# Kernel optimization log

Measured on AMD Instinct MI355X. Metric: run time of the kernel, lower is better.

The kernel has to match this reference:

```python
import jax, jax.numpy as jnp
import numpy as np

FEAT = 64      # feature_dim
HEADS = 4      # n_head
LATENT = 256   # latent_dim
G = 128        # num graphs
NPG = 150      # nodes per graph (<=180 for one-hot positions)
N = G * NPG    # 19200 nodes
E = N * 12     # 230400 edges (excl. self loops)
POS = 180      # one-hot position classes
SLOPE = 0.2    # PyG GATConv leaky_relu negative slope


def gat_conv(x, src, dst, W, att_s, att_d, bias):
    """PyG GATConv (concat heads, self loops already appended to src/dst)."""
    n = x.shape[0]
    h = (x @ W).reshape(n, HEADS, FEAT)                 # [N,H,F]
    a_s = jnp.sum(h * att_s, axis=-1)                   # [N,H]
    a_d = jnp.sum(h * att_d, axis=-1)                   # [N,H]
    e = jax.nn.leaky_relu(a_s[src] + a_d[dst], SLOPE)   # [E,H] per-edge logits
    m = jax.ops.segment_max(e, dst, num_segments=n)     # segment softmax over dst
    ex = jnp.exp(e - m[dst])
    s = jax.ops.segment_sum(ex, dst, num_segments=n)
    alpha = ex / (s[dst] + 1e-16)
    out = jax.ops.segment_sum(h[src] * alpha[:, :, None], dst, num_segments=n)
    return out.reshape(n, HEADS * FEAT) + bias


def setup_inputs() -> dict:
    key = jax.random.key(0)
    ks = jax.random.split(key, 20)

    def p(k, shape, fan_in):
        return jax.random.normal(k, shape, jnp.float32) / np.sqrt(fan_in).astype(np.float32)

    z = jax.random.normal(ks[0], (G, LATENT), jnp.float32)
    src = jax.random.randint(ks[1], (E,), 0, N, jnp.int32)
    dst = (src + jax.random.randint(ks[2], (E,), 1, N, jnp.int32)) % N  # no self loops
    edge_index = jnp.stack([src, dst])
    batch = jnp.repeat(jnp.arange(G, dtype=jnp.int32), NPG)

    in1 = FEAT + POS
    in2 = FEAT * HEADS
    inp = dict(z=z, edge_index=edge_index, batch=batch, num_graphs=G)
    inp.update(
        W0=p(ks[3], (LATENT, FEAT), LATENT), b0=jnp.zeros(FEAT, jnp.float32),
        W1=p(ks[4], (in1, HEADS * FEAT), in1),
        as1=p(ks[5], (HEADS, FEAT), FEAT), ad1=p(ks[6], (HEADS, FEAT), FEAT),
        bb1=jnp.zeros(HEADS * FEAT, jnp.float32),
        W2=p(ks[7], (in2, HEADS * FEAT), in2),
        as2=p(ks[8], (HEADS, FEAT), FEAT), ad2=p(ks[9], (HEADS, FEAT), FEAT),
        bb2=jnp.zeros(HEADS * FEAT, jnp.float32),
        W3=p(ks[10], (in2, HEADS * FEAT), in2),
        as3=p(ks[11], (HEADS, FEAT), FEAT), ad3=p(ks[12], (HEADS, FEAT), FEAT),
        bb3=jnp.zeros(HEADS * FEAT, jnp.float32),
        Wg=p(ks[13], (in2, FEAT), in2), bg=jnp.zeros(FEAT, jnp.float32),
        Wf=p(ks[14], (FEAT, 5), FEAT), bf=jnp.zeros(5, jnp.float32),
    )
    return inp


def reference(z, edge_index, batch, num_graphs,
              W0, b0, W1, as1, ad1, bb1, W2, as2, ad2, bb2,
              W3, as3, ad3, bb3, Wg, bg, Wf, bf):
    n = batch.shape[0]
    x = z @ W0 + b0                                    # dec_feature_init
    x = x[batch]                                       # broadcast graph latent to nodes
    # node_order_within_batch (batch is sorted)
    counts = jax.ops.segment_sum(jnp.ones_like(batch), batch, num_segments=num_graphs)
    starts = jnp.cumsum(counts) - counts
    order = jnp.arange(n, dtype=batch.dtype) - starts[batch]
    pos = jax.nn.one_hot(order, POS, dtype=x.dtype)
    x = jax.nn.relu(jnp.concatenate([x, pos], axis=1))
    # GATConv adds self loops by default
    loops = jnp.arange(n, dtype=edge_index.dtype)
    src = jnp.concatenate([edge_index[0], loops])
    dst = jnp.concatenate([edge_index[1], loops])
    x = jax.nn.relu(gat_conv(x, src, dst, W1, as1, ad1, bb1))
    x = jax.nn.relu(gat_conv(x, src, dst, W2, as2, ad2, bb2))
    x = jax.nn.relu(gat_conv(x, src, dst, W3, as3, ad3, bb3))
    x = jax.nn.relu(x @ Wg + bg)                       # dec_geo
    return x @ Wf + bf                                 # fc_geo -> [N,5]
```

## Files before the change

kernel.cpp:

```cpp
#include <hip/hip_runtime.h>
#include <hip/hip_fp16.h>

#define GNUM 128
#define HEADS 4
#define FEAT 64
#define CH 256
#define LAT 256
#define SLOPE 0.2f
#define CAP 64
#define POSMAX 180

typedef _Float16 h16;
typedef __attribute__((ext_vector_type(4))) _Float16 half4;
typedef __attribute__((ext_vector_type(8))) _Float16 half8;
typedef __attribute__((ext_vector_type(4))) float floatx4;

__device__ __forceinline__ float lrelu(float x) { return fmaxf(x, SLOPE * x); }

__global__ __launch_bounds__(256) void k_setup(const int* __restrict__ batch, int* __restrict__ cnt,
                                               int* __restrict__ starts, int n,
                                               const float* __restrict__ W2, const float* __restrict__ W3,
                                               const float* __restrict__ Wg, h16* __restrict__ W2T,
                                               h16* __restrict__ W3T, h16* __restrict__ WgT,
                                               const float* __restrict__ z, const float* __restrict__ W0,
                                               const float* __restrict__ b0, const float* __restrict__ W1,
                                               const float* __restrict__ as1, const float* __restrict__ ad1,
                                               float* __restrict__ A, float* __restrict__ asg,
                                               float* __restrict__ adg, float* __restrict__ asp,
                                               float* __restrict__ adp) {
  __shared__ float red[4][FEAT];
  __shared__ float xzs[FEAT];
  int bx = blockIdx.x, t = threadIdx.x;
  if (bx < 576) {
    int idx = bx * 256 + t;
    if (idx < n) {
      cnt[idx] = 0;
      int b = batch[idx];
      if (idx == 0 || batch[idx - 1] != b) starts[b] = idx;
    }
    if (idx < 65536) {
      int kb = idx >> 13, rem = idx & 8191, j = rem >> 8, nn = rem & 255;
      W2T[kb * 8192 + nn * 32 + j] = (h16)W2[(kb * 32 + j) * 256 + nn];
    } else if (idx < 131072) {
      int l = idx - 65536;
      int kb = l >> 13, rem = l & 8191, j = rem >> 8, nn = rem & 255;
      W3T[kb * 8192 + nn * 32 + j] = (h16)W3[(kb * 32 + j) * 256 + nn];
    } else {
      int l = idx - 131072;
      int kb = l >> 11, rem = l & 2047, j = rem >> 6, nn = rem & 63;
      WgT[kb * 2048 + nn * 32 + j] = (h16)Wg[(kb * 32 + j) * 64 + nn];
    }
  } else if (bx < 576 + GNUM) {
    int g = bx - 576;
    int f = t & 63, kq = t >> 6;
    float acc = 0.f;
    for (int k = kq * 64; k < kq * 64 + 64; ++k) acc += z[g * LAT + k] * W0[k * FEAT + f];
    red[kq][f] = acc;
    __syncthreads();
    if (kq == 0)
      xzs[f] = fmaxf(red[0][f] + red[1][f] + red[2][f] + red[3][f] + b0[f], 0.f);
    __syncthreads();
    float a2 = 0.f;
#pragma unroll 16
    for (int k = 0; k < FEAT; ++k) a2 += xzs[k] * W1[k * CH + t];
    A[g * CH + t] = a2;
    float ps = a2 * as1[t], pd = a2 * ad1[t];
#pragma unroll
    for (int sh = 1; sh < 64; sh <<= 1) {
      ps += __shfl_xor(ps, sh, 64);
      pd += __shfl_xor(pd, sh, 64);
    }
    if ((t & 63) == 0) {
      asg[g * 4 + (t >> 6)] = ps;
      adg[g * 4 + (t >> 6)] = pd;
    }
  } else {
    int p = bx - (576 + GNUM);
    float wv = W1[(size_t)(FEAT + p) * CH + t];
    float ps = wv * as1[t], pd = wv * ad1[t];
#pragma unroll
    for (int sh = 1; sh < 64; sh <<= 1) {
      ps += __shfl_xor(ps, sh, 64);
      pd += __shfl_xor(pd, sh, 64);
    }
    if ((t & 63) == 0) {
      asp[p * 4 + (t >> 6)] = ps;
      adp[p * 4 + (t >> 6)] = pd;
    }
  }
}

__global__ __launch_bounds__(256) void k_pre(const float* __restrict__ A, const float* __restrict__ W1,
                                             const int* __restrict__ batch, const int* __restrict__ starts,
                                             const float* __restrict__ asg, const float* __restrict__ adg,
                                             const float* __restrict__ asp, const float* __restrict__ adp,
                                             h16* __restrict__ H16, float* __restrict__ a_s,
                                             float* __restrict__ a_d, int n,
                                             const int* __restrict__ src, const int* __restrict__ dst,
                                             int* __restrict__ cnt, int* __restrict__ bucket, int e,
                                             int h1blocks) {
  int t = threadIdx.x;
  if ((int)blockIdx.x < h1blocks) {
    int row = blockIdx.x * 8 + (t >> 5);
    if (row < n) {
      int g = batch[row];
      int p = row - starts[g];
      int c0 = (t & 31) * 8;
      const float* ap = A + g * CH + c0;
      const float* wp = W1 + (size_t)(FEAT + p) * CH + c0;
      float4 a0 = *(const float4*)ap;
      float4 a1 = *(const float4*)(ap + 4);
      float4 w0v = *(const float4*)wp;
      float4 w1v = *(const float4*)(wp + 4);
      half8 o;
      o[0] = (h16)(a0.x + w0v.x); o[1] = (h16)(a0.y + w0v.y);
      o[2] = (h16)(a0.z + w0v.z); o[3] = (h16)(a0.w + w0v.w);
      o[4] = (h16)(a1.x + w1v.x); o[5] = (h16)(a1.y + w1v.y);
      o[6] = (h16)(a1.z + w1v.z); o[7] = (h16)(a1.w + w1v.w);
      *(half8*)(H16 + (size_t)row * CH + c0) = o;
    }
    int idx = blockIdx.x * 256 + t;
    if (idx < n * 4) {
      int nn = idx >> 2, h = idx & 3;
      int g2 = batch[nn], p2 = nn - starts[g2];
      a_s[idx] = asg[g2 * 4 + h] + asp[p2 * 4 + h];
      a_d[idx] = adg[g2 * 4 + h] + adp[p2 * 4 + h];
    }
  } else {
    int i = (blockIdx.x - h1blocks) * 256 + t;
    if (i < e) {
      int d = dst[i];
      int p = atomicAdd(&cnt[d], 1);
      if (p < CAP) bucket[d * CAP + p] = src[i];
    }
  }
}

__global__ __launch_bounds__(256) void k_galpha(const h16* __restrict__ H16, const float* __restrict__ a_s,
                                                const float* __restrict__ a_d, const float* __restrict__ bias,
                                                const int* __restrict__ cnt, const int* __restrict__ bucket,
                                                h16* __restrict__ X16) {
  __shared__ float wsh[4][CAP][4];
  __shared__ int bsh[4][CAP];
  int wv = threadIdx.x >> 6, lane = threadIdx.x & 63;
  int n = blockIdx.x * 4 + wv;
  int c = min(cnt[n], CAP);
  bool valid = lane < c;
  int sc = valid ? bucket[n * CAP + lane] : n;
  if (valid) bsh[wv][lane] = sc;
  float4 ea4 = *(const float4*)(a_s + (size_t)sc * 4);
  float4 sn4 = *(const float4*)(a_s + (size_t)n * 4);
  float4 dn4 = *(const float4*)(a_d + (size_t)n * 4);
  float ea[4] = {ea4.x, ea4.y, ea4.z, ea4.w};
  float sn[4] = {sn4.x, sn4.y, sn4.z, sn4.w};
  float dn[4] = {dn4.x, dn4.y, dn4.z, dn4.w};
  float asf[4];
#pragma unroll
  for (int h = 0; h < 4; ++h) {
    float e = valid ? lrelu(ea[h] + dn[h]) : -1e30f;
    float es = lrelu(sn[h] + dn[h]);
    float m = e;
#pragma unroll
    for (int sh = 1; sh < 64; sh <<= 1) m = fmaxf(m, __shfl_xor(m, sh, 64));
    m = fmaxf(m, es);
    float wgt = valid ? __expf(e - m) : 0.f;
    float ws = __expf(es - m);
    float s = wgt;
#pragma unroll
    for (int sh = 1; sh < 64; sh <<= 1) s += __shfl_xor(s, sh, 64);
    s += ws;
    float inv = 1.f / (s + 1e-16f);
    if (valid) wsh[wv][lane][h] = wgt * inv;
    asf[h] = ws * inv;
  }
  int hh = lane >> 4;
  int fo = lane * 4;
  half4 hv = *(const half4*)(H16 + (size_t)n * CH + fo);
  float a_self = asf[hh];
  float acc0 = a_self * (float)hv[0];
  float acc1 = a_self * (float)hv[1];
  float acc2 = a_self * (float)hv[2];
  float acc3 = a_self * (float)hv[3];
#define GLD(k) (*(const half4*)(H16 + (size_t)bsh[wv][k] * CH + fo))
  half4 q0, q1, q2, q3, q4, q5, q6, q7;
  if (c > 0) q0 = GLD(0);
  if (c > 1) q1 = GLD(1);
  if (c > 2) q2 = GLD(2);
  if (c > 3) q3 = GLD(3);
  if (c > 4) q4 = GLD(4);
  if (c > 5) q5 = GLD(5);
  if (c > 6) q6 = GLD(6);
  if (c > 7) q7 = GLD(7);
  for (int j0 = 0; j0 < c; j0 += 8) {
#define STEP(K, QK)                                              \
    if (j0 + K < c) {                                            \
      float wj = wsh[wv][j0 + K][hh];                            \
      half4 hc = QK;                                             \
      if (j0 + K + 8 < c) QK = GLD(j0 + K + 8);                  \
      acc0 += wj * (float)hc[0];                                 \
      acc1 += wj * (float)hc[1];                                 \
      acc2 += wj * (float)hc[2];                                 \
      acc3 += wj * (float)hc[3];                                 \
    }
    STEP(0, q0) STEP(1, q1) STEP(2, q2) STEP(3, q3)
    STEP(4, q4) STEP(5, q5) STEP(6, q6) STEP(7, q7)
#undef STEP
  }
#undef GLD
  float4 b4 = *(const float4*)(bias + fo);
  half4 o;
  o[0] = (h16)fmaxf(acc0 + b4.x, 0.f);
  o[1] = (h16)fmaxf(acc1 + b4.y, 0.f);
  o[2] = (h16)fmaxf(acc2 + b4.z, 0.f);
  o[3] = (h16)fmaxf(acc3 + b4.w, 0.f);
  *(half4*)(X16 + (size_t)n * CH + fo) = o;
}

__global__ __launch_bounds__(256) void k_gemm(const h16* __restrict__ X16, const h16* __restrict__ WT,
                                              const float* __restrict__ att_s, const float* __restrict__ att_d,
                                              h16* __restrict__ H16, float* __restrict__ a_s,
                                              float* __restrict__ a_d) {
  __shared__ __align__(16) char smem[80 * 264 * 2];
  h16* As = (h16*)smem;
  h16* Bs = (h16*)(smem + 6400);
  h16* Ht = (h16*)smem;
  int t = threadIdx.x;
  int w = t >> 6, lane = t & 63;
  int quad = lane >> 4, l15 = lane & 15;
  int row0 = blockIdx.x * 80;
  int arow = t >> 2, aseg = t & 3;
  floatx4 acc[5][4];
#pragma unroll
  for (int i = 0; i < 5; ++i)
#pragma unroll
    for (int j = 0; j < 4; ++j) acc[i][j] = (floatx4){0.f, 0.f, 0.f, 0.f};
  half8 ra0, ra1, rb0, rb1, rb2, rb3;
  ra0 = *(const half8*)(X16 + (size_t)(row0 + arow) * CH + aseg * 8);
  if (t < 64) ra1 = *(const half8*)(X16 + (size_t)(row0 + arow + 64) * CH + aseg * 8);
  {
    const h16* s = WT + t * 32;
    rb0 = *(const half8*)(s + 0);  rb1 = *(const half8*)(s + 8);
    rb2 = *(const half8*)(s + 16); rb3 = *(const half8*)(s + 24);
  }
  for (int kb = 0; kb < 8; ++kb) {
    __syncthreads();
    *(half8*)&As[arow * 40 + aseg * 8] = ra0;
    if (t < 64) *(half8*)&As[(arow + 64) * 40 + aseg * 8] = ra1;
    {
      h16* bd = &Bs[t * 40];
      *(half8*)(bd + 0) = rb0;  *(half8*)(bd + 8) = rb1;
      *(half8*)(bd + 16) = rb2; *(half8*)(bd + 24) = rb3;
    }
    __syncthreads();
    if (kb < 7) {
      ra0 = *(const half8*)(X16 + (size_t)(row0 + arow) * CH + (kb + 1) * 32 + aseg * 8);
      if (t < 64)
        ra1 = *(const half8*)(X16 + (size_t)(row0 + arow + 64) * CH + (kb + 1) * 32 + aseg * 8);
      const h16* s = WT + (kb + 1) * 8192 + t * 32;
      rb0 = *(const half8*)(s + 0);  rb1 = *(const half8*)(s + 8);
      rb2 = *(const half8*)(s + 16); rb3 = *(const half8*)(s + 24);
    }
    half8 af[5], bf[4];
#pragma unroll
    for (int mt = 0; mt < 5; ++mt) af[mt] = *(const half8*)&As[(mt * 16 + l15) * 40 + quad * 8];
#pragma unroll
    for (int nt = 0; nt < 4; ++nt)
      bf[nt] = *(const half8*)&Bs[(w * 64 + nt * 16 + l15) * 40 + quad * 8];
#pragma unroll
    for (int mt = 0; mt < 5; ++mt)
#pragma unroll
      for (int nt = 0; nt < 4; ++nt)
        acc[mt][nt] = __builtin_amdgcn_mfma_f32_16x16x32_f16(af[mt], bf[nt], acc[mt][nt], 0, 0, 0);
  }
  __syncthreads();
#pragma unroll
  for (int mt = 0; mt < 5; ++mt)
#pragma unroll
    for (int nt = 0; nt < 4; ++nt)
#pragma unroll
      for (int r = 0; r < 4; ++r)
        Ht[(mt * 16 + quad * 4 + r) * 264 + w * 64 + nt * 16 + l15] = (h16)acc[mt][nt][r];
  float asv[4], adv[4];
#pragma unroll
  for (int nt = 0; nt < 4; ++nt) {
    asv[nt] = att_s[w * FEAT + nt * 16 + l15];
    adv[nt] = att_d[w * FEAT + nt * 16 + l15];
  }
#pragma unroll
  for (int mt = 0; mt < 5; ++mt)
#pragma unroll
    for (int r = 0; r < 4; ++r) {
      float ps = acc[mt][0][r] * asv[0] + acc[mt][1][r] * asv[1] +
                 acc[mt][2][r] * asv[2] + acc[mt][3][r] * asv[3];
      float pd = acc[mt][0][r] * adv[0] + acc[mt][1][r] * adv[1] +
                 acc[mt][2][r] * adv[2] + acc[mt][3][r] * adv[3];
#pragma unroll
      for (int sh = 1; sh < 16; sh <<= 1) {
        ps += __shfl_xor(ps, sh, 16);
        pd += __shfl_xor(pd, sh, 16);
      }
      if (l15 == 0) {
        int row = row0 + mt * 16 + quad * 4 + r;
        a_s[row * 4 + w] = ps;
        a_d[row * 4 + w] = pd;
      }
    }
  __syncthreads();
  for (int rr = t >> 2; rr < 80; rr += 64) {
    const h16* srcr = &Ht[rr * 264 + aseg * 64];
    h16* dstr = H16 + (size_t)(row0 + rr) * CH + aseg * 64;
#pragma unroll
    for (int i = 0; i < 8; ++i) *(half8*)(dstr + i * 8) = *(const half8*)(srcr + i * 8);
  }
}

__global__ __launch_bounds__(256) void k_head(const h16* __restrict__ X16, const h16* __restrict__ WgT,
                                              const float* __restrict__ bg, const float* __restrict__ Wf,
                                              const float* __restrict__ bfv, float* __restrict__ out) {
  __shared__ __align__(16) char smem[80 * 68 * 4];
  h16* As = (h16*)smem;
  h16* Bs = (h16*)(smem + 6400);
  float* ytile = (float*)smem;
  __shared__ float WfS[FEAT * 5];
  int t = threadIdx.x;
  int w = t >> 6, lane = t & 63;
  int quad = lane >> 4, l15 = lane & 15;
  int row0 = blockIdx.x * 80;
  int arow = t >> 2, aseg = t & 3;
  for (int i = t; i < FEAT * 5; i += 256) WfS[i] = Wf[i];
  floatx4 acc[5];
#pragma unroll
  for (int mt = 0; mt < 5; ++mt) acc[mt] = (floatx4){0.f, 0.f, 0.f, 0.f};
  half8 ra0, ra1, rb;
  ra0 = *(const half8*)(X16 + (size_t)(row0 + arow) * CH + aseg * 8);
  if (t < 64) ra1 = *(const half8*)(X16 + (size_t)(row0 + arow + 64) * CH + aseg * 8);
  rb = *(const half8*)(WgT + arow * 32 + aseg * 8);
  for (int kb = 0; kb < 8; ++kb) {
    __syncthreads();
    *(half8*)&As[arow * 40 + aseg * 8] = ra0;
    if (t < 64) *(half8*)&As[(arow + 64) * 40 + aseg * 8] = ra1;
    *(half8*)&Bs[arow * 40 + aseg * 8] = rb;
    __syncthreads();
    if (kb < 7) {
      ra0 = *(const half8*)(X16 + (size_t)(row0 + arow) * CH + (kb + 1) * 32 + aseg * 8);
      if (t < 64)
        ra1 = *(const half8*)(X16 + (size_t)(row0 + arow + 64) * CH + (kb + 1) * 32 + aseg * 8);
      rb = *(const half8*)(WgT + (kb + 1) * 2048 + arow * 32 + aseg * 8);
    }
    half8 af[5], bfr;
#pragma unroll
    for (int mt = 0; mt < 5; ++mt) af[mt] = *(const half8*)&As[(mt * 16 + l15) * 40 + quad * 8];
    bfr = *(const half8*)&Bs[(w * 16 + l15) * 40 + quad * 8];
#pragma unroll
    for (int mt = 0; mt < 5; ++mt)
      acc[mt] = __builtin_amdgcn_mfma_f32_16x16x32_f16(af[mt], bfr, acc[mt], 0, 0, 0);
  }
  __syncthreads();
  int col = w * 16 + l15;
  float bgv = bg[col];
#pragma unroll
  for (int mt = 0; mt < 5; ++mt)
#pragma unroll
    for (int r = 0; r < 4; ++r)
      ytile[(mt * 16 + quad * 4 + r) * 68 + col] = fmaxf(acc[mt][r] + bgv, 0.f);
  __syncthreads();
  for (int i = t; i < 80 * 5; i += 256) {
    int row = i / 5, o = i % 5;
    float s = bfv[o];
#pragma unroll
    for (int k = 0; k < FEAT; ++k) s += ytile[row * 68 + k] * WfS[k * 5 + o];
    out[(size_t)(row0 + row) * 5 + o] = s;
  }
}

static inline size_t alignup(size_t x) { return (x + 255) & ~(size_t)255; }

extern "C" void kernel_launch(void* const* d_in, const int* in_sizes, int n_in,
                              void* d_out, int out_size, void* d_ws, size_t ws_size,
                              hipStream_t stream) {
  (void)n_in; (void)out_size; (void)ws_size;
  const float* z   = (const float*)d_in[0];
  const int* edge  = (const int*)d_in[1];
  const int* batch = (const int*)d_in[2];
  const float* W0  = (const float*)d_in[4];
  const float* b0  = (const float*)d_in[5];
  const float* W1  = (const float*)d_in[6];
  const float* as1 = (const float*)d_in[7];
  const float* ad1 = (const float*)d_in[8];
  const float* bb1 = (const float*)d_in[9];
  const float* W2  = (const float*)d_in[10];
  const float* as2 = (const float*)d_in[11];
  const float* ad2 = (const float*)d_in[12];
  const float* bb2 = (const float*)d_in[13];
  const float* W3  = (const float*)d_in[14];
  const float* as3 = (const float*)d_in[15];
  const float* ad3 = (const float*)d_in[16];
  const float* bb3 = (const float*)d_in[17];
  const float* Wg  = (const float*)d_in[18];
  const float* bg  = (const float*)d_in[19];
  const float* Wf  = (const float*)d_in[20];
  const float* bfv = (const float*)d_in[21];
  float* out = (float*)d_out;

  const int E = in_sizes[1] / 2;
  const int N = in_sizes[2];
  const int* srcI = edge;
  const int* dstI = edge + E;

  char* w = (char*)d_ws;
  auto carve = [&](size_t bytes) { void* p = (void*)w; w += alignup(bytes); return p; };
  int* starts  = (int*)carve((size_t)GNUM * 4);
  int* cnt     = (int*)carve((size_t)N * 4);
  int* bucket  = (int*)carve((size_t)N * CAP * 4);
  float* A     = (float*)carve((size_t)GNUM * CH * 4);
  float* a_s   = (float*)carve((size_t)N * 4 * 4);
  float* a_d   = (float*)carve((size_t)N * 4 * 4);
  float* asg   = (float*)carve((size_t)GNUM * 4 * 4);
  float* adg   = (float*)carve((size_t)GNUM * 4 * 4);
  float* asp   = (float*)carve((size_t)POSMAX * 4 * 4);
  float* adp   = (float*)carve((size_t)POSMAX * 4 * 4);
  h16* W2T     = (h16*)carve((size_t)CH * CH * 2);
  h16* W3T     = (h16*)carve((size_t)CH * CH * 2);
  h16* WgT     = (h16*)carve((size_t)CH * FEAT * 2);
  h16* H16     = (h16*)carve((size_t)N * CH * 2);
  h16* X16     = (h16*)carve((size_t)N * CH * 2);

  int h1blocks = N / 8;
  int ebl = (E + 255) / 256;

  hipLaunchKernelGGL(k_setup, dim3(576 + GNUM + POSMAX), dim3(256), 0, stream,
                     batch, cnt, starts, N, W2, W3, Wg, W2T, W3T, WgT, z, W0, b0, W1,
                     as1, ad1, A, asg, adg, asp, adp);
  hipLaunchKernelGGL(k_pre, dim3(h1blocks + ebl), dim3(256), 0, stream,
                     A, W1, batch, starts, asg, adg, asp, adp, H16, a_s, a_d, N,
                     srcI, dstI, cnt, bucket, E, h1blocks);
  hipLaunchKernelGGL(k_galpha, dim3(N / 4), dim3(256), 0, stream, H16, a_s, a_d, bb1, cnt, bucket, X16);
  hipLaunchKernelGGL(k_gemm, dim3(N / 80), dim3(256), 0, stream, X16, W2T, as2, ad2, H16, a_s, a_d);
  hipLaunchKernelGGL(k_galpha, dim3(N / 4), dim3(256), 0, stream, H16, a_s, a_d, bb2, cnt, bucket, X16);
  hipLaunchKernelGGL(k_gemm, dim3(N / 80), dim3(256), 0, stream, X16, W3T, as3, ad3, H16, a_s, a_d);
  hipLaunchKernelGGL(k_galpha, dim3(N / 4), dim3(256), 0, stream, H16, a_s, a_d, bb3, cnt, bucket, X16);
  hipLaunchKernelGGL(k_head, dim3(N / 80), dim3(256), 0, stream, X16, WgT, bg, Wf, bfv, out);
}
```

Before: 270.1 us.

## Store head-major H and map heads to XCDs in GAT aggregation

Changes the projected feature buffer to a head-major layout ([head][node][64]) written by both the pre-kernel and the GEMM epilogue. The aggregation kernel now launches one block per (head, node-quad) pair, with the block index decoded so each pair of XCDs handles one head. Each of those L2 caches then only sees a quarter of H. Within a wave, four 16-lane groups gather different neighbours in parallel and are combined by shuffle reduction, with the next gather prefetched. The aim is higher L2 hit rate and better memory-level parallelism for the random neighbour gathers. The cost is 4x more blocks, each wave redoing the softmax for its head, and a reliance on a block-to-XCD round-robin assumption.

```diff
diff --git a/kernel.cpp b/kernel.cpp
--- a/kernel.cpp
+++ b/kernel.cpp
@@ -94,7 +94,7 @@
                                              const int* __restrict__ batch, const int* __restrict__ starts,
                                              const float* __restrict__ asg, const float* __restrict__ adg,
                                              const float* __restrict__ asp, const float* __restrict__ adp,
-                                             h16* __restrict__ H16, float* __restrict__ a_s,
+                                             h16* __restrict__ Hh, float* __restrict__ a_s,
                                              float* __restrict__ a_d, int n,
                                              const int* __restrict__ src, const int* __restrict__ dst,
                                              int* __restrict__ cnt, int* __restrict__ bucket, int e,
@@ -117,7 +117,7 @@
       o[2] = (h16)(a0.z + w0v.z); o[3] = (h16)(a0.w + w0v.w);
       o[4] = (h16)(a1.x + w1v.x); o[5] = (h16)(a1.y + w1v.y);
       o[6] = (h16)(a1.z + w1v.z); o[7] = (h16)(a1.w + w1v.w);
-      *(half8*)(H16 + (size_t)row * CH + c0) = o;
+      *(half8*)(Hh + ((size_t)(c0 >> 6) * n + row) * 64 + (c0 & 63)) = o;
     }
     int idx = blockIdx.x * 256 + t;
     if (idx < n * 4) {
@@ -136,90 +136,77 @@
   }
 }
 
-__global__ __launch_bounds__(256) void k_galpha(const h16* __restrict__ H16, const float* __restrict__ a_s,
-                                                const float* __restrict__ a_d, const float* __restrict__ bias,
-                                                const int* __restrict__ cnt, const int* __restrict__ bucket,
-                                                h16* __restrict__ X16) {
-  __shared__ float wsh[4][CAP][4];
-  __shared__ int bsh[4][CAP];
-  int wv = threadIdx.x >> 6, lane = threadIdx.x & 63;
-  int n = blockIdx.x * 4 + wv;
+__global__ __launch_bounds__(256) void k_gat(const h16* __restrict__ Hh, const float* __restrict__ a_s,
+                                             const float* __restrict__ a_d, const float* __restrict__ bias,
+                                             const int* __restrict__ cnt, const int* __restrict__ bucket,
+                                             h16* __restrict__ X16, int nn) {
+  int t = threadIdx.x, wv = t >> 6, lane = t & 63;
+  int b = blockIdx.x;
+  int xcd = b & 7, q = b >> 3;
+  int head = xcd >> 1, p = xcd & 1;
+  int n = p * (nn >> 1) + q * 4 + wv;
+  int grp = lane >> 4, l15 = lane & 15;
+  const h16* H = Hh + (size_t)head * nn * 64;
   int c = min(cnt[n], CAP);
   bool valid = lane < c;
-  int sc = valid ? bucket[n * CAP + lane] : n;
-  if (valid) bsh[wv][lane] = sc;
-  float4 ea4 = *(const float4*)(a_s + (size_t)sc * 4);
-  float4 sn4 = *(const float4*)(a_s + (size_t)n * 4);
-  float4 dn4 = *(const float4*)(a_d + (size_t)n * 4);
-  float ea[4] = {ea4.x, ea4.y, ea4.z, ea4.w};
-  float sn[4] = {sn4.x, sn4.y, sn4.z, sn4.w};
-  float dn[4] = {dn4.x, dn4.y, dn4.z, dn4.w};
-  float asf[4];
-#pragma unroll
-  for (int h = 0; h < 4; ++h) {
-    float e = valid ? lrelu(ea[h] + dn[h]) : -1e30f;
-    float es = lrelu(sn[h] + dn[h]);
-    float m = e;
-#pragma unroll
-    for (int sh = 1; sh < 64; sh <<= 1) m = fmaxf(m, __shfl_xor(m, sh, 64));
-    m = fmaxf(m, es);
-    float wgt = valid ? __expf(e - m) : 0.f;
-    float ws = __expf(es - m);
-    float s = wgt;
-#pragma unroll
-    for (int sh = 1; sh < 64; sh <<= 1) s += __shfl_xor(s, sh, 64);
-    s += ws;
-    float inv = 1.f / (s + 1e-16f);
-    if (valid) wsh[wv][lane][h] = wgt * inv;
-    asf[h] = ws * inv;
-  }
-  int hh = lane >> 4;
-  int fo = lane * 4;
-  half4 hv = *(const half4*)(H16 + (size_t)n * CH + fo);
-  float a_self = asf[hh];
-  float acc0 = a_self * (float)hv[0];
-  float acc1 = a_self * (float)hv[1];
-  float acc2 = a_self * (float)hv[2];
-  float acc3 = a_self * (float)hv[3];
-#define GLD(k) (*(const half4*)(H16 + (size_t)bsh[wv][k] * CH + fo))
-  half4 q0, q1, q2, q3, q4, q5, q6, q7;
-  if (c > 0) q0 = GLD(0);
-  if (c > 1) q1 = GLD(1);
-  if (c > 2) q2 = GLD(2);
-  if (c > 3) q3 = GLD(3);
-  if (c > 4) q4 = GLD(4);
-  if (c > 5) q5 = GLD(5);
-  if (c > 6) q6 = GLD(6);
-  if (c > 7) q7 = GLD(7);
-  for (int j0 = 0; j0 < c; j0 += 8) {
-#define STEP(K, QK)                                              \
-    if (j0 + K < c) {                                            \
-      float wj = wsh[wv][j0 + K][hh];                            \
-      half4 hc = QK;                                             \
-      if (j0 + K + 8 < c) QK = GLD(j0 + K + 8);                  \
-      acc0 += wj * (float)hc[0];                                 \
-      acc1 += wj * (float)hc[1];                                 \
-      acc2 += wj * (float)hc[2];                                 \
-      acc3 += wj * (float)hc[3];                                 \
-    }
-    STEP(0, q0) STEP(1, q1) STEP(2, q2) STEP(3, q3)
-    STEP(4, q4) STEP(5, q5) STEP(6, q6) STEP(7, q7)
-#undef STEP
-  }
-#undef GLD
-  float4 b4 = *(const float4*)(bias + fo);
-  half4 o;
-  o[0] = (h16)fmaxf(acc0 + b4.x, 0.f);
-  o[1] = (h16)fmaxf(acc1 + b4.y, 0.f);
-  o[2] = (h16)fmaxf(acc2 + b4.z, 0.f);
-  o[3] = (h16)fmaxf(acc3 + b4.w, 0.f);
-  *(half4*)(X16 + (size_t)n * CH + fo) = o;
+  int src_l = valid ? bucket[n * CAP + lane] : n;
+  float dn = a_d[n * 4 + head];
+  float e_l = valid ? lrelu(a_s[src_l * 4 + head] + dn) : -1e30f;
+  float es = lrelu(a_s[n * 4 + head] + dn);
+  float m = e_l;
+#pragma unroll
+  for (int sh = 1; sh < 64; sh <<= 1) m = fmaxf(m, __shfl_xor(m, sh, 64));
+  m = fmaxf(m, es);
+  float wgt = valid ? __expf(e_l - m) : 0.f;
+  float ws = __expf(es - m);
+  float s = wgt;
+#pragma unroll
+  for (int sh = 1; sh < 64; sh <<= 1) s += __shfl_xor(s, sh, 64);
+  s += ws;
+  float inv = 1.f / (s + 1e-16f);
+  wgt *= inv;
+  ws *= inv;
+  float acc0 = 0.f, acc1 = 0.f, acc2 = 0.f, acc3 = 0.f;
+  int steps = (c + 4) >> 2;
+  int jj = grp - 1;
+  int s0 = __shfl(src_l, jj < 0 ? 0 : (jj & 63), 64);
+  int sA = (jj < 0) ? n : s0;
+  half4 fA = *(const half4*)(H + (size_t)sA * 64 + l15 * 4);
+  for (int it = 0; it < steps; ++it) {
+    int jn = jj + 4;
+    half4 fB;
+    if (it + 1 < steps) {
+      int sB = __shfl(src_l, jn & 63, 64);
+      fB = *(const half4*)(H + (size_t)sB * 64 + l15 * 4);
+    }
+    float wb = __shfl(wgt, (jj < 0 ? 0 : jj) & 63, 64);
+    float w = (jj < 0) ? ws : ((jj < c) ? wb : 0.f);
+    acc0 += w * (float)fA[0];
+    acc1 += w * (float)fA[1];
+    acc2 += w * (float)fA[2];
+    acc3 += w * (float)fA[3];
+    fA = fB;
+    jj = jn;
+  }
+  acc0 += __shfl_xor(acc0, 16, 64); acc0 += __shfl_xor(acc0, 32, 64);
+  acc1 += __shfl_xor(acc1, 16, 64); acc1 += __shfl_xor(acc1, 32, 64);
+  acc2 += __shfl_xor(acc2, 16, 64); acc2 += __shfl_xor(acc2, 32, 64);
+  acc3 += __shfl_xor(acc3, 16, 64); acc3 += __shfl_xor(acc3, 32, 64);
+  if (grp == 0) {
+    float4 b4 = *(const float4*)(bias + head * 64 + l15 * 4);
+    half4 o;
+    o[0] = (h16)fmaxf(acc0 + b4.x, 0.f);
+    o[1] = (h16)fmaxf(acc1 + b4.y, 0.f);
+    o[2] = (h16)fmaxf(acc2 + b4.z, 0.f);
+    o[3] = (h16)fmaxf(acc3 + b4.w, 0.f);
+    *(half4*)(X16 + (size_t)n * CH + head * 64 + l15 * 4) = o;
+  }
 }
 
 __global__ __launch_bounds__(256) void k_gemm(const h16* __restrict__ X16, const h16* __restrict__ WT,
                                               const float* __restrict__ att_s, const float* __restrict__ att_d,
-                                              h16* __restrict__ H16, float* __restrict__ a_s,
-                                              float* __restrict__ a_d) {
+                                              h16* __restrict__ Hh, float* __restrict__ a_s,
+                                              float* __restrict__ a_d, int nn) {
   __shared__ __align__(16) char smem[80 * 264 * 2];
   h16* As = (h16*)smem;
   h16* Bs = (h16*)(smem + 6400);
@@ -308,7 +295,7 @@
   __syncthreads();
   for (int rr = t >> 2; rr < 80; rr += 64) {
     const h16* srcr = &Ht[rr * 264 + aseg * 64];
-    h16* dstr = H16 + (size_t)(row0 + rr) * CH + aseg * 64;
+    h16* dstr = Hh + ((size_t)aseg * nn + row0 + rr) * 64;
 #pragma unroll
     for (int i = 0; i < 8; ++i) *(half8*)(dstr + i * 8) = *(const half8*)(srcr + i * 8);
   }
@@ -422,7 +409,7 @@
   h16* W2T     = (h16*)carve((size_t)CH * CH * 2);
   h16* W3T     = (h16*)carve((size_t)CH * CH * 2);
   h16* WgT     = (h16*)carve((size_t)CH * FEAT * 2);
-  h16* H16     = (h16*)carve((size_t)N * CH * 2);
+  h16* Hh      = (h16*)carve((size_t)N * CH * 2);
   h16* X16     = (h16*)carve((size_t)N * CH * 2);
 
   int h1blocks = N / 8;
@@ -432,12 +419,12 @@
                      batch, cnt, starts, N, W2, W3, Wg, W2T, W3T, WgT, z, W0, b0, W1,
                      as1, ad1, A, asg, adg, asp, adp);
   hipLaunchKernelGGL(k_pre, dim3(h1blocks + ebl), dim3(256), 0, stream,
-                     A, W1, batch, starts, asg, adg, asp, adp, H16, a_s, a_d, N,
+                     A, W1, batch, starts, asg, adg, asp, adp, Hh, a_s, a_d, N,
                      srcI, dstI, cnt, bucket, E, h1blocks);
-  hipLaunchKernelGGL(k_galpha, dim3(N / 4), dim3(256), 0, stream, H16, a_s, a_d, bb1, cnt, bucket, X16);
-  hipLaunchKernelGGL(k_gemm, dim3(N / 80), dim3(256), 0, stream, X16, W2T, as2, ad2, H16, a_s, a_d);
-  hipLaunchKernelGGL(k_galpha, dim3(N / 4), dim3(256), 0, stream, H16, a_s, a_d, bb2, cnt, bucket, X16);
-  hipLaunchKernelGGL(k_gemm, dim3(N / 80), dim3(256), 0, stream, X16, W3T, as3, ad3, H16, a_s, a_d);
-  hipLaunchKernelGGL(k_galpha, dim3(N / 4), dim3(256), 0, stream, H16, a_s, a_d, bb3, cnt, bucket, X16);
+  hipLaunchKernelGGL(k_gat, dim3(N), dim3(256), 0, stream, Hh, a_s, a_d, bb1, cnt, bucket, X16, N);
+  hipLaunchKernelGGL(k_gemm, dim3(N / 80), dim3(256), 0, stream, X16, W2T, as2, ad2, Hh, a_s, a_d, N);
+  hipLaunchKernelGGL(k_gat, dim3(N), dim3(256), 0, stream, Hh, a_s, a_d, bb2, cnt, bucket, X16, N);
+  hipLaunchKernelGGL(k_gemm, dim3(N / 80), dim3(256), 0, stream, X16, W3T, as3, ad3, Hh, a_s, a_d, N);
+  hipLaunchKernelGGL(k_gat, dim3(N), dim3(256), 0, stream, Hh, a_s, a_d, bb3, cnt, bucket, X16, N);
   hipLaunchKernelGGL(k_head, dim3(N / 80), dim3(256), 0, stream, X16, WgT, bg, Wf, bfv, out);
 }
```

Result: slower. 297.8 us (+10.3%).

## Fuse all stages into one cooperative persistent kernel with grid syncs

Applied to the files above, without the earlier changes.

Replaces the eight separate kernel launches with a single cooperative persistent kernel. It walks through setup, preprocessing, three GAT aggregation phases, two GEMMs and the head, separated by grid.sync. This removes per-launch overhead and the idle gaps between kernels. In exchange the grid is capped at occupancy-derived blocks using grid-stride work loops, so each phase may get less parallelism than before and each grid barrier has its own cost. The old multi-launch path is kept as a fallback if the cooperative launch fails.

```diff
diff --git a/kernel.cpp b/kernel.cpp
--- a/kernel.cpp
+++ b/kernel.cpp
@@ -1,5 +1,8 @@
 #include <hip/hip_runtime.h>
 #include <hip/hip_fp16.h>
+#include <hip/hip_cooperative_groups.h>
+
+namespace cg = cooperative_groups;
 
 #define GNUM 128
 #define HEADS 4
@@ -16,6 +19,335 @@
 typedef __attribute__((ext_vector_type(4))) float floatx4;
 
 __device__ __forceinline__ float lrelu(float x) { return fmaxf(x, SLOPE * x); }
+
+
+__device__ __forceinline__ void gat_phase(const h16* __restrict__ H16, const float* __restrict__ a_s,
+                                          const float* __restrict__ a_d, const float* __restrict__ bias,
+                                          const int* __restrict__ cnt, const int* __restrict__ bucket,
+                                          h16* __restrict__ X16, int nn, int gw, int gws) {
+  __shared__ float wsh[4][CAP][4];
+  __shared__ int bsh[4][CAP];
+  int wv = threadIdx.x >> 6, lane = threadIdx.x & 63;
+  int hh = lane >> 4, fo = lane * 4;
+  for (int n = gw; n < nn; n += gws) {
+    int c = min(cnt[n], CAP);
+    bool valid = lane < c;
+    int sc = valid ? bucket[n * CAP + lane] : n;
+    if (valid) bsh[wv][lane] = sc;
+    float4 ea4 = *(const float4*)(a_s + (size_t)sc * 4);
+    float4 sn4 = *(const float4*)(a_s + (size_t)n * 4);
+    float4 dn4 = *(const float4*)(a_d + (size_t)n * 4);
+    float ea[4] = {ea4.x, ea4.y, ea4.z, ea4.w};
+    float sn[4] = {sn4.x, sn4.y, sn4.z, sn4.w};
+    float dn[4] = {dn4.x, dn4.y, dn4.z, dn4.w};
+    float asf[4];
+#pragma unroll
+    for (int h = 0; h < 4; ++h) {
+      float e = valid ? lrelu(ea[h] + dn[h]) : -1e30f;
+      float es = lrelu(sn[h] + dn[h]);
+      float m = e;
+#pragma unroll
+      for (int sh = 1; sh < 64; sh <<= 1) m = fmaxf(m, __shfl_xor(m, sh, 64));
+      m = fmaxf(m, es);
+      float wgt = valid ? __expf(e - m) : 0.f;
+      float ws = __expf(es - m);
+      float s = wgt;
+#pragma unroll
+      for (int sh = 1; sh < 64; sh <<= 1) s += __shfl_xor(s, sh, 64);
+      s += ws;
+      float inv = 1.f / (s + 1e-16f);
+      if (valid) wsh[wv][lane][h] = wgt * inv;
+      asf[h] = ws * inv;
+    }
+    half4 hv = *(const half4*)(H16 + (size_t)n * CH + fo);
+    float a_self = asf[hh];
+    float acc0 = a_self * (float)hv[0];
+    float acc1 = a_self * (float)hv[1];
+    float acc2 = a_self * (float)hv[2];
+    float acc3 = a_self * (float)hv[3];
+#define GLD(k) (*(const half4*)(H16 + (size_t)bsh[wv][k] * CH + fo))
+    half4 q0, q1, q2, q3, q4, q5, q6, q7;
+    if (c > 0) q0 = GLD(0);
+    if (c > 1) q1 = GLD(1);
+    if (c > 2) q2 = GLD(2);
+    if (c > 3) q3 = GLD(3);
+    if (c > 4) q4 = GLD(4);
+    if (c > 5) q5 = GLD(5);
+    if (c > 6) q6 = GLD(6);
+    if (c > 7) q7 = GLD(7);
+    for (int j0 = 0; j0 < c; j0 += 8) {
+#define STEP(K, QK)                                              \
+      if (j0 + K < c) {                                          \
+        float wj = wsh[wv][j0 + K][hh];                          \
+        half4 hc = QK;                                           \
+        if (j0 + K + 8 < c) QK = GLD(j0 + K + 8);                \
+        acc0 += wj * (float)hc[0];                               \
+        acc1 += wj * (float)hc[1];                               \
+        acc2 += wj * (float)hc[2];                               \
+        acc3 += wj * (float)hc[3];                               \
+      }
+      STEP(0, q0) STEP(1, q1) STEP(2, q2) STEP(3, q3)
+      STEP(4, q4) STEP(5, q5) STEP(6, q6) STEP(7, q7)
+#undef STEP
+    }
+#undef GLD
+    float4 b4 = *(const float4*)(bias + fo);
+    half4 o;
+    o[0] = (h16)fmaxf(acc0 + b4.x, 0.f);
+    o[1] = (h16)fmaxf(acc1 + b4.y, 0.f);
+    o[2] = (h16)fmaxf(acc2 + b4.z, 0.f);
+    o[3] = (h16)fmaxf(acc3 + b4.w, 0.f);
+    *(half4*)(X16 + (size_t)n * CH + fo) = o;
+  }
+}
+
+__device__ __forceinline__ void gemm_phase(const h16* __restrict__ X16, const h16* __restrict__ WT,
+                                           const float* __restrict__ att_s, const float* __restrict__ att_d,
+                                           h16* __restrict__ H16, float* __restrict__ a_s,
+                                           float* __restrict__ a_d, int nn, int gw, int gws) {
+  int lane = threadIdx.x & 63, quad = lane >> 4, l15 = lane & 15;
+  int items = (nn >> 4) << 2;
+  for (int it = gw; it < items; it += gws) {
+    int tile = it >> 2, s = it & 3;
+    int row0 = tile << 4;
+    const h16* ap = X16 + (size_t)(row0 + l15) * CH + quad * 8;
+    const h16* bp = WT + (s * 64 + l15) * 32 + quad * 8;
+    floatx4 acc0 = {0.f, 0.f, 0.f, 0.f}, acc1 = acc0, acc2 = acc0, acc3 = acc0;
+#pragma unroll 2
+    for (int kb = 0; kb < 8; ++kb) {
+      half8 af = *(const half8*)(ap + kb * 32);
+      half8 b0 = *(const half8*)(bp + kb * 8192);
+      half8 b1 = *(const half8*)(bp + kb * 8192 + 512);
+      half8 b2 = *(const half8*)(bp + kb * 8192 + 1024);
+      half8 b3 = *(const half8*)(bp + kb * 8192 + 1536);
+      acc0 = __builtin_amdgcn_mfma_f32_16x16x32_f16(af, b0, acc0, 0, 0, 0);
+      acc1 = __builtin_amdgcn_mfma_f32_16x16x32_f16(af, b1, acc1, 0, 0, 0);
+      acc2 = __builtin_amdgcn_mfma_f32_16x16x32_f16(af, b2, acc2, 0, 0, 0);
+      acc3 = __builtin_amdgcn_mfma_f32_16x16x32_f16(af, b3, acc3, 0, 0, 0);
+    }
+    float asv[4], adv[4];
+#pragma unroll
+    for (int nt = 0; nt < 4; ++nt) {
+      asv[nt] = att_s[s * FEAT + nt * 16 + l15];
+      adv[nt] = att_d[s * FEAT + nt * 16 + l15];
+    }
+#pragma unroll
+    for (int r = 0; r < 4; ++r) {
+      float ps = acc0[r] * asv[0] + acc1[r] * asv[1] + acc2[r] * asv[2] + acc3[r] * asv[3];
+      float pd = acc0[r] * adv[0] + acc1[r] * adv[1] + acc2[r] * adv[2] + acc3[r] * adv[3];
+#pragma unroll
+      for (int sh = 1; sh < 16; sh <<= 1) {
+        ps += __shfl_xor(ps, sh, 16);
+        pd += __shfl_xor(pd, sh, 16);
+      }
+      if (l15 == 0) {
+        int row = row0 + quad * 4 + r;
+        a_s[row * 4 + s] = ps;
+        a_d[row * 4 + s] = pd;
+      }
+    }
+    h16* hp = H16 + (size_t)row0 * CH + s * 64 + l15;
+#pragma unroll
+    for (int r = 0; r < 4; ++r) {
+      size_t ro = (size_t)(quad * 4 + r) * CH;
+      hp[ro]      = (h16)acc0[r];
+      hp[ro + 16] = (h16)acc1[r];
+      hp[ro + 32] = (h16)acc2[r];
+      hp[ro + 48] = (h16)acc3[r];
+    }
+  }
+}
+
+__device__ __forceinline__ void head_phase(const h16* __restrict__ X16, const h16* __restrict__ WgT,
+                                           const float* __restrict__ bg, const float* __restrict__ Wf,
+                                           const float* __restrict__ bfv, float* __restrict__ out,
+                                           int nn, int gw, int gws) {
+  int lane = threadIdx.x & 63, quad = lane >> 4, l15 = lane & 15;
+  int items = nn >> 4;
+  for (int it = gw; it < items; it += gws) {
+    int row0 = it << 4;
+    const h16* ap = X16 + (size_t)(row0 + l15) * CH + quad * 8;
+    const h16* bp = WgT + l15 * 32 + quad * 8;
+    floatx4 acc0 = {0.f, 0.f, 0.f, 0.f}, acc1 = acc0, acc2 = acc0, acc3 = acc0;
+#pragma unroll 2
+    for (int kb = 0; kb < 8; ++kb) {
+      half8 af = *(const half8*)(ap + kb * 32);
+      half8 b0 = *(const half8*)(bp + kb * 2048);
+      half8 b1 = *(const half8*)(bp + kb * 2048 + 512);
+      half8 b2 = *(const half8*)(bp + kb * 2048 + 1024);
+      half8 b3 = *(const half8*)(bp + kb * 2048 + 1536);
+      acc0 = __builtin_amdgcn_mfma_f32_16x16x32_f16(af, b0, acc0, 0, 0, 0);
+      acc1 = __builtin_amdgcn_mfma_f32_16x16x32_f16(af, b1, acc1, 0, 0, 0);
+      acc2 = __builtin_amdgcn_mfma_f32_16x16x32_f16(af, b2, acc2, 0, 0, 0);
+      acc3 = __builtin_amdgcn_mfma_f32_16x16x32_f16(af, b3, acc3, 0, 0, 0);
+    }
+    float g0 = bg[l15], g1 = bg[16 + l15], g2 = bg[32 + l15], g3 = bg[48 + l15];
+    float y0[4], y1[4], y2[4], y3[4];
+#pragma unroll
+    for (int r = 0; r < 4; ++r) {
+      y0[r] = fmaxf(acc0[r] + g0, 0.f);
+      y1[r] = fmaxf(acc1[r] + g1, 0.f);
+      y2[r] = fmaxf(acc2[r] + g2, 0.f);
+      y3[r] = fmaxf(acc3[r] + g3, 0.f);
+    }
+    float wf0[5], wf1[5], wf2[5], wf3[5];
+#pragma unroll
+    for (int o = 0; o < 5; ++o) {
+      wf0[o] = Wf[l15 * 5 + o];
+      wf1[o] = Wf[(16 + l15) * 5 + o];
+      wf2[o] = Wf[(32 + l15) * 5 + o];
+      wf3[o] = Wf[(48 + l15) * 5 + o];
+    }
+#pragma unroll
+    for (int r = 0; r < 4; ++r)
+#pragma unroll
+      for (int o = 0; o < 5; ++o) {
+        float p = y0[r] * wf0[o] + y1[r] * wf1[o] + y2[r] * wf2[o] + y3[r] * wf3[o];
+        p += __shfl_xor(p, 1, 16);
+        p += __shfl_xor(p, 2, 16);
+        p += __shfl_xor(p, 4, 16);
+        p += __shfl_xor(p, 8, 16);
+        if (l15 == 0) out[(size_t)(row0 + quad * 4 + r) * 5 + o] = p + bfv[o];
+      }
+  }
+}
+
+struct MegaArgs {
+  const int *batch, *src, *dst;
+  int nn, e;
+  const float *z, *W0, *b0, *W1, *as1, *ad1, *bb1;
+  const float *W2, *as2, *ad2, *bb2, *W3, *as3, *ad3, *bb3;
+  const float *Wg, *bg, *Wf, *bfv;
+  float* out;
+  int *starts, *cnt, *bucket;
+  float *A, *a_s, *a_d, *asg, *adg, *asp, *adp;
+  h16 *W2T, *W3T, *WgT, *H16, *X16;
+};
+
+__global__ __launch_bounds__(256, 6) void k_mega(MegaArgs a) {
+  cg::grid_group grid = cg::this_grid();
+  int t = threadIdx.x;
+  int nb = gridDim.x;
+  int gw = blockIdx.x * 4 + (t >> 6), gws = nb * 4;
+
+  {
+    __shared__ float red[4][FEAT];
+    __shared__ float xzs[FEAT];
+    for (int v = blockIdx.x; v < 576 + GNUM + POSMAX; v += nb) {
+      if (v < 576) {
+        int idx = v * 256 + t;
+        if (idx < a.nn) {
+          a.cnt[idx] = 0;
+          int b = a.batch[idx];
+          if (idx == 0 || a.batch[idx - 1] != b) a.starts[b] = idx;
+        }
+        if (idx < 65536) {
+          int kb = idx >> 13, rem = idx & 8191, j = rem >> 8, c = rem & 255;
+          a.W2T[kb * 8192 + c * 32 + j] = (h16)a.W2[(kb * 32 + j) * 256 + c];
+        } else if (idx < 131072) {
+          int l = idx - 65536;
+          int kb = l >> 13, rem = l & 8191, j = rem >> 8, c = rem & 255;
+          a.W3T[kb * 8192 + c * 32 + j] = (h16)a.W3[(kb * 32 + j) * 256 + c];
+        } else {
+          int l = idx - 131072;
+          int kb = l >> 11, rem = l & 2047, j = rem >> 6, c = rem & 63;
+          a.WgT[kb * 2048 + c * 32 + j] = (h16)a.Wg[(kb * 32 + j) * 64 + c];
+        }
+      } else if (v < 576 + GNUM) {
+        int g = v - 576;
+        int f = t & 63, kq = t >> 6;
+        float acc = 0.f;
+        for (int k = kq * 64; k < kq * 64 + 64; ++k) acc += a.z[g * LAT + k] * a.W0[k * FEAT + f];
+        red[kq][f] = acc;
+        __syncthreads();
+        if (kq == 0)
+          xzs[f] = fmaxf(red[0][f] + red[1][f] + red[2][f] + red[3][f] + a.b0[f], 0.f);
+        __syncthreads();
+        float a2 = 0.f;
+#pragma unroll 16
+        for (int k = 0; k < FEAT; ++k) a2 += xzs[k] * a.W1[k * CH + t];
+        a.A[g * CH + t] = a2;
+        float ps = a2 * a.as1[t], pd = a2 * a.ad1[t];
+#pragma unroll
+        for (int sh = 1; sh < 64; sh <<= 1) {
+          ps += __shfl_xor(ps, sh, 64);
+          pd += __shfl_xor(pd, sh, 64);
+        }
+        if ((t & 63) == 0) {
+          a.asg[g * 4 + (t >> 6)] = ps;
+          a.adg[g * 4 + (t >> 6)] = pd;
+        }
+      } else {
+        int p = v - (576 + GNUM);
+        float wv1 = a.W1[(size_t)(FEAT + p) * CH + t];
+        float ps = wv1 * a.as1[t], pd = wv1 * a.ad1[t];
+#pragma unroll
+        for (int sh = 1; sh < 64; sh <<= 1) {
+          ps += __shfl_xor(ps, sh, 64);
+          pd += __shfl_xor(pd, sh, 64);
+        }
+        if ((t & 63) == 0) {
+          a.asp[p * 4 + (t >> 6)] = ps;
+          a.adp[p * 4 + (t >> 6)] = pd;
+        }
+      }
+    }
+  }
+  grid.sync();
+  {
+    int h1v = a.nn >> 3;
+    int ev = (a.e + 255) >> 8;
+    for (int v = blockIdx.x; v < h1v + ev; v += nb) {
+      if (v < h1v) {
+        int row = v * 8 + (t >> 5);
+        if (row < a.nn) {
+          int g = a.batch[row];
+          int p = row - a.starts[g];
+          int c0 = (t & 31) * 8;
+          const float* ap = a.A + g * CH + c0;
+          const float* wp = a.W1 + (size_t)(FEAT + p) * CH + c0;
+          float4 a0 = *(const float4*)ap;
+          float4 a1 = *(const float4*)(ap + 4);
+          float4 w0v = *(const float4*)wp;
+          float4 w1v = *(const float4*)(wp + 4);
+          half8 o;
+          o[0] = (h16)(a0.x + w0v.x); o[1] = (h16)(a0.y + w0v.y);
+          o[2] = (h16)(a0.z + w0v.z); o[3] = (h16)(a0.w + w0v.w);
+          o[4] = (h16)(a1.x + w1v.x); o[5] = (h16)(a1.y + w1v.y);
+          o[6] = (h16)(a1.z + w1v.z); o[7] = (h16)(a1.w + w1v.w);
+          *(half8*)(a.H16 + (size_t)row * CH + c0) = o;
+        }
+        int idx = v * 256 + t;
+        if (idx < a.nn * 4) {
+          int n2 = idx >> 2, h = idx & 3;
+          int g2 = a.batch[n2], p2 = n2 - a.starts[g2];
+          a.a_s[idx] = a.asg[g2 * 4 + h] + a.asp[p2 * 4 + h];
+          a.a_d[idx] = a.adg[g2 * 4 + h] + a.adp[p2 * 4 + h];
+        }
+      } else {
+        int i = (v - h1v) * 256 + t;
+        if (i < a.e) {
+          int d = a.dst[i];
+          int p = atomicAdd(&a.cnt[d], 1);
+          if (p < CAP) a.bucket[d * CAP + p] = a.src[i];
+        }
+      }
+    }
+  }
+  grid.sync();
+  gat_phase(a.H16, a.a_s, a.a_d, a.bb1, a.cnt, a.bucket, a.X16, a.nn, gw, gws);
+  grid.sync();
+  gemm_phase(a.X16, a.W2T, a.as2, a.ad2, a.H16, a.a_s, a.a_d, a.nn, gw, gws);
+  grid.sync();
+  gat_phase(a.H16, a.a_s, a.a_d, a.bb2, a.cnt, a.bucket, a.X16, a.nn, gw, gws);
+  grid.sync();
+  gemm_phase(a.X16, a.W3T, a.as3, a.ad3, a.H16, a.a_s, a.a_d, a.nn, gw, gws);
+  grid.sync();
+  gat_phase(a.H16, a.a_s, a.a_d, a.bb3, a.cnt, a.bucket, a.X16, a.nn, gw, gws);
+  grid.sync();
+  head_phase(a.X16, a.WgT, a.bg, a.Wf, a.bfv, a.out, a.nn, gw, gws);
+}
+
 
 __global__ __launch_bounds__(256) void k_setup(const int* __restrict__ batch, int* __restrict__ cnt,
                                                int* __restrict__ starts, int n,
@@ -425,9 +757,29 @@
   h16* H16     = (h16*)carve((size_t)N * CH * 2);
   h16* X16     = (h16*)carve((size_t)N * CH * 2);
 
+  MegaArgs ma;
+  ma.batch = batch; ma.src = srcI; ma.dst = dstI; ma.nn = N; ma.e = E;
+  ma.z = z; ma.W0 = W0; ma.b0 = b0; ma.W1 = W1; ma.as1 = as1; ma.ad1 = ad1; ma.bb1 = bb1;
+  ma.W2 = W2; ma.as2 = as2; ma.ad2 = ad2; ma.bb2 = bb2;
+  ma.W3 = W3; ma.as3 = as3; ma.ad3 = ad3; ma.bb3 = bb3;
+  ma.Wg = Wg; ma.bg = bg; ma.Wf = Wf; ma.bfv = bfv; ma.out = out;
+  ma.starts = starts; ma.cnt = cnt; ma.bucket = bucket;
+  ma.A = A; ma.a_s = a_s; ma.a_d = a_d;
+  ma.asg = asg; ma.adg = adg; ma.asp = asp; ma.adp = adp;
+  ma.W2T = W2T; ma.W3T = W3T; ma.WgT = WgT; ma.H16 = H16; ma.X16 = X16;
+
+  int nbpm = 0;
+  hipError_t oe = hipOccupancyMaxActiveBlocksPerMultiprocessor(&nbpm, k_mega, 256, 0);
+  if (oe != hipSuccess || nbpm < 1) nbpm = 4;
+  if (nbpm > 8) nbpm = 8;
+  int gridsz = nbpm * 256;
+  void* kargs[] = {(void*)&ma};
+  hipError_t le = hipLaunchCooperativeKernel(k_mega, dim3(gridsz), dim3(256), kargs, 0, stream);
+  if (le == hipSuccess) return;
+
+  (void)hipGetLastError();
   int h1blocks = N / 8;
   int ebl = (E + 255) / 256;
-
   hipLaunchKernelGGL(k_setup, dim3(576 + GNUM + POSMAX), dim3(256), 0, stream,
                      batch, cnt, starts, N, W2, W3, Wg, W2T, W3T, WgT, z, W0, b0, W1,
                      as1, ad1, A, asg, adg, asp, adp);
```

Measured after the change: 1.004 ms. 3.72x slower.

## Split GAT aggregation per node across two wavefronts, each handling two heads

Applied to the files above, without the earlier changes.

The attention aggregation kernel now assigns two wavefronts to each destination node, each covering two heads and half the feature channels with 2-element half loads, and doubles the grid size. The gather prefetch depth is raised from 8 to 16 neighbor rows. The aim is more parallelism and more memory requests in flight for the latency-bound neighbor gather. In exchange, each neighbor's indices and logits are reloaded by two waves, and the narrower 4-byte loads use fewer bytes per request.

```diff
diff --git a/kernel.cpp b/kernel.cpp
--- a/kernel.cpp
+++ b/kernel.cpp
@@ -11,6 +11,7 @@
 #define POSMAX 180
 
 typedef _Float16 h16;
+typedef __attribute__((ext_vector_type(2))) _Float16 h162;
 typedef __attribute__((ext_vector_type(4))) _Float16 half4;
 typedef __attribute__((ext_vector_type(8))) _Float16 half8;
 typedef __attribute__((ext_vector_type(4))) float floatx4;
@@ -140,23 +141,24 @@
                                                 const float* __restrict__ a_d, const float* __restrict__ bias,
                                                 const int* __restrict__ cnt, const int* __restrict__ bucket,
                                                 h16* __restrict__ X16) {
-  __shared__ float wsh[4][CAP][4];
+  __shared__ float wsh[4][CAP][2];
   __shared__ int bsh[4][CAP];
   int wv = threadIdx.x >> 6, lane = threadIdx.x & 63;
-  int n = blockIdx.x * 4 + wv;
+  int n = blockIdx.x * 2 + (wv >> 1);
+  int hf = wv & 1;
   int c = min(cnt[n], CAP);
   bool valid = lane < c;
   int sc = valid ? bucket[n * CAP + lane] : n;
   if (valid) bsh[wv][lane] = sc;
-  float4 ea4 = *(const float4*)(a_s + (size_t)sc * 4);
-  float4 sn4 = *(const float4*)(a_s + (size_t)n * 4);
-  float4 dn4 = *(const float4*)(a_d + (size_t)n * 4);
-  float ea[4] = {ea4.x, ea4.y, ea4.z, ea4.w};
-  float sn[4] = {sn4.x, sn4.y, sn4.z, sn4.w};
-  float dn[4] = {dn4.x, dn4.y, dn4.z, dn4.w};
-  float asf[4];
-#pragma unroll
-  for (int h = 0; h < 4; ++h) {
+  float2 ea2 = *(const float2*)(a_s + (size_t)sc * 4 + hf * 2);
+  float2 sn2 = *(const float2*)(a_s + (size_t)n * 4 + hf * 2);
+  float2 dn2 = *(const float2*)(a_d + (size_t)n * 4 + hf * 2);
+  float ea[2] = {ea2.x, ea2.y};
+  float sn[2] = {sn2.x, sn2.y};
+  float dn[2] = {dn2.x, dn2.y};
+  float asf[2];
+#pragma unroll
+  for (int h = 0; h < 2; ++h) {
     float e = valid ? lrelu(ea[h] + dn[h]) : -1e30f;
     float es = lrelu(sn[h] + dn[h]);
     float m = e;
@@ -173,47 +175,51 @@
     if (valid) wsh[wv][lane][h] = wgt * inv;
     asf[h] = ws * inv;
   }
-  int hh = lane >> 4;
-  int fo = lane * 4;
-  half4 hv = *(const half4*)(H16 + (size_t)n * CH + fo);
+  int hh = lane >> 5;
+  int fo = hf * 128 + lane * 2;
+  h162 hv = *(const h162*)(H16 + (size_t)n * CH + fo);
   float a_self = asf[hh];
   float acc0 = a_self * (float)hv[0];
   float acc1 = a_self * (float)hv[1];
-  float acc2 = a_self * (float)hv[2];
-  float acc3 = a_self * (float)hv[3];
-#define GLD(k) (*(const half4*)(H16 + (size_t)bsh[wv][k] * CH + fo))
-  half4 q0, q1, q2, q3, q4, q5, q6, q7;
-  if (c > 0) q0 = GLD(0);
-  if (c > 1) q1 = GLD(1);
-  if (c > 2) q2 = GLD(2);
-  if (c > 3) q3 = GLD(3);
-  if (c > 4) q4 = GLD(4);
-  if (c > 5) q5 = GLD(5);
-  if (c > 6) q6 = GLD(6);
-  if (c > 7) q7 = GLD(7);
-  for (int j0 = 0; j0 < c; j0 += 8) {
+#define GLD(k) (*(const h162*)(H16 + (size_t)bsh[wv][k] * CH + fo))
+  h162 q0, q1, q2, q3, q4, q5, q6, q7, q8, q9, q10, q11, q12, q13, q14, q15;
+  if (c > 0)  q0  = GLD(0);
+  if (c > 1)  q1  = GLD(1);
+  if (c > 2)  q2  = GLD(2);
+  if (c > 3)  q3  = GLD(3);
+  if (c > 4)  q4  = GLD(4);
+  if (c > 5)  q5  = GLD(5);
+  if (c > 6)  q6  = GLD(6);
+  if (c > 7)  q7  = GLD(7);
+  if (c > 8)  q8  = GLD(8);
+  if (c > 9)  q9  = GLD(9);
+  if (c > 10) q10 = GLD(10);
+  if (c > 11) q11 = GLD(11);
+  if (c > 12) q12 = GLD(12);
+  if (c > 13) q13 = GLD(13);
+  if (c > 14) q14 = GLD(14);
+  if (c > 15) q15 = GLD(15);
+  for (int j0 = 0; j0 < c; j0 += 16) {
 #define STEP(K, QK)                                              \
     if (j0 + K < c) {                                            \
       float wj = wsh[wv][j0 + K][hh];                            \
-      half4 hc = QK;                                             \
-      if (j0 + K + 8 < c) QK = GLD(j0 + K + 8);                  \
+      h162 hc = QK;                                              \
+      if (j0 + K + 16 < c) QK = GLD(j0 + K + 16);                \
       acc0 += wj * (float)hc[0];                                 \
       acc1 += wj * (float)hc[1];                                 \
-      acc2 += wj * (float)hc[2];                                 \
-      acc3 += wj * (float)hc[3];                                 \
-    }
-    STEP(0, q0) STEP(1, q1) STEP(2, q2) STEP(3, q3)
-    STEP(4, q4) STEP(5, q5) STEP(6, q6) STEP(7, q7)
+    }
+    STEP(0, q0)  STEP(1, q1)  STEP(2, q2)  STEP(3, q3)
+    STEP(4, q4)  STEP(5, q5)  STEP(6, q6)  STEP(7, q7)
+    STEP(8, q8)  STEP(9, q9)  STEP(10, q10) STEP(11, q11)
+    STEP(12, q12) STEP(13, q13) STEP(14, q14) STEP(15, q15)
 #undef STEP
   }
 #undef GLD
-  float4 b4 = *(const float4*)(bias + fo);
-  half4 o;
-  o[0] = (h16)fmaxf(acc0 + b4.x, 0.f);
-  o[1] = (h16)fmaxf(acc1 + b4.y, 0.f);
-  o[2] = (h16)fmaxf(acc2 + b4.z, 0.f);
-  o[3] = (h16)fmaxf(acc3 + b4.w, 0.f);
-  *(half4*)(X16 + (size_t)n * CH + fo) = o;
+  float2 b2 = *(const float2*)(bias + fo);
+  h162 o;
+  o[0] = (h16)fmaxf(acc0 + b2.x, 0.f);
+  o[1] = (h16)fmaxf(acc1 + b2.y, 0.f);
+  *(h162*)(X16 + (size_t)n * CH + fo) = o;
 }
 
 __global__ __launch_bounds__(256) void k_gemm(const h16* __restrict__ X16, const h16* __restrict__ WT,
@@ -434,10 +440,10 @@
   hipLaunchKernelGGL(k_pre, dim3(h1blocks + ebl), dim3(256), 0, stream,
                      A, W1, batch, starts, asg, adg, asp, adp, H16, a_s, a_d, N,
                      srcI, dstI, cnt, bucket, E, h1blocks);
-  hipLaunchKernelGGL(k_galpha, dim3(N / 4), dim3(256), 0, stream, H16, a_s, a_d, bb1, cnt, bucket, X16);
+  hipLaunchKernelGGL(k_galpha, dim3(N / 2), dim3(256), 0, stream, H16, a_s, a_d, bb1, cnt, bucket, X16);
   hipLaunchKernelGGL(k_gemm, dim3(N / 80), dim3(256), 0, stream, X16, W2T, as2, ad2, H16, a_s, a_d);
-  hipLaunchKernelGGL(k_galpha, dim3(N / 4), dim3(256), 0, stream, H16, a_s, a_d, bb2, cnt, bucket, X16);
+  hipLaunchKernelGGL(k_galpha, dim3(N / 2), dim3(256), 0, stream, H16, a_s, a_d, bb2, cnt, bucket, X16);
   hipLaunchKernelGGL(k_gemm, dim3(N / 80), dim3(256), 0, stream, X16, W3T, as3, ad3, H16, a_s, a_d);
-  hipLaunchKernelGGL(k_galpha, dim3(N / 4), dim3(256), 0, stream, H16, a_s, a_d, bb3, cnt, bucket, X16);
+  hipLaunchKernelGGL(k_galpha, dim3(N / 2), dim3(256), 0, stream, H16, a_s, a_d, bb3, cnt, bucket, X16);
   hipLaunchKernelGGL(k_head, dim3(N / 80), dim3(256), 0, stream, X16, WgT, bg, Wf, bfv, out);
 }
```

Result: slower. 286.4 us (+6.0%).
